# Kernel optimization log

Hardware: AMD Instinct MI355X
Metric: run time of the kernel (lower is better)

## Reference

```python
import jax, jax.numpy as jnp
import numpy as np

D_MODEL = 1024
HIDDEN = 4096
N_EXPERTS = 8
TOP_K = 2


def setup_inputs() -> dict:
    key = jax.random.key(0)
    ks = jax.random.split(key, 7)
    x = jax.random.normal(ks[0], (4, 2048, D_MODEL), dtype=jnp.float32)
    s = 0.02
    Wg = jax.random.normal(ks[1], (D_MODEL, N_EXPERTS), dtype=jnp.float32) * s
    bg = jnp.zeros((N_EXPERTS,), dtype=jnp.float32)
    W1 = jax.random.normal(ks[2], (N_EXPERTS, D_MODEL, HIDDEN), dtype=jnp.float32) * s
    b1 = jnp.zeros((N_EXPERTS, HIDDEN), dtype=jnp.float32)
    W2 = jax.random.normal(ks[3], (N_EXPERTS, HIDDEN, D_MODEL), dtype=jnp.float32) * s
    b2 = jnp.zeros((N_EXPERTS, D_MODEL), dtype=jnp.float32)
    return {"x": x, "Wg": Wg, "bg": bg, "W1": W1, "b1": b1, "W2": W2, "b2": b2}


def reference(x, Wg, bg, W1, b1, W2, b2):
    B, T, D = x.shape
    xf = x.reshape(-1, D)                      # (N, D)
    N = xf.shape[0]

    # --- top-k gate ---
    logits = xf @ Wg + bg                      # (N, E)
    all_probs = jax.nn.softmax(logits, axis=-1)
    topk_logits, topk_idx = jax.lax.top_k(logits, TOP_K)   # (N, k)
    topk_gates = jax.nn.softmax(topk_logits, axis=-1)      # (N, k), sums to 1

    # scatter gates into dense (N, E) masks (matches torch scatter_add_)
    rows = jnp.arange(N)[:, None]
    gate_mask = jnp.zeros((N, N_EXPERTS), dtype=xf.dtype).at[rows, topk_idx].add(topk_gates)
    dispatch_mask = jnp.zeros((N, N_EXPERTS), dtype=xf.dtype).at[rows, topk_idx].add(1.0)

    # --- experts: dense batched form; unselected tokens have gate 0 so math matches ---
    h = jnp.einsum('nd,edh->neh', xf, W1) + b1             # (N, E, H)
    h = jax.nn.relu(h)
    y = jnp.einsum('neh,ehd->ned', h, W2) + b2             # (N, E, D)
    out = jnp.einsum('ned,ne->nd', y, gate_mask)           # weighted combine
    outputs = out.reshape(B, T, D)

    # --- load-balance loss + metadata ---
    tokens_per_expert = (dispatch_mask > 0).sum(axis=0)
    assignment_fraction = gate_mask.sum(axis=0) / N
    expected_prob = all_probs.mean(axis=0)
    load_balance_loss = (expected_prob * assignment_fraction).sum() * N_EXPERTS

    return (outputs, load_balance_loss, tokens_per_expert, expected_prob, assignment_fraction)
```

## Files before the change

### kernel.cpp

```cpp
#include <hip/hip_runtime.h>
#include <stdint.h>

#define D_MODEL 1024
#define HID     4096
#define NE      8
#define NTOK    8192
#define NSLOT   (NTOK*2)
#define TM      128
#define MAX_RB  136
#define MPAD    (MAX_RB*TM)
#define HHALF   2048
#define GATE_BLOCKS 256

typedef unsigned short u16;
typedef __attribute__((ext_vector_type(8))) __bf16 bf16x8;
typedef __attribute__((ext_vector_type(4))) float  f32x4;

__device__ __forceinline__ u16 f2bu(float f){
  uint32_t u = __builtin_bit_cast(uint32_t, f);
  uint32_t r = (u + 0x7FFFu + ((u >> 16) & 1u)) >> 16;
  return (u16)r;
}
__device__ __forceinline__ float b2f(u16 v){
  uint32_t u = ((uint32_t)v) << 16;
  return __builtin_bit_cast(float, u);
}

__device__ __forceinline__ void gload16(const u16* src, u16* lds){
  __builtin_amdgcn_global_load_lds((const __attribute__((address_space(1))) void*)src,
                                   (__attribute__((address_space(3))) void*)lds, 16, 0, 0);
}

__device__ __forceinline__ int xcd_swz(int w, int nwg){
  int q = nwg >> 3;
  return (w & 7) * q + (w >> 3);
}

#define WAITV(n) do{ asm volatile("s_waitcnt vmcnt(" #n ")" ::: "memory"); \
                     __builtin_amdgcn_sched_barrier(0); }while(0)
#define BARX()   do{ __builtin_amdgcn_sched_barrier(0); \
                     __builtin_amdgcn_s_barrier(); \
                     __builtin_amdgcn_sched_barrier(0); }while(0)

__global__ __launch_bounds__(256) void transpose_cvt(const float* __restrict__ in,
                                                     u16* __restrict__ out, int R, int C)
{
  __shared__ float tile[64][33];
  int e = blockIdx.z;
  int r0 = blockIdx.y * 64, c0 = blockIdx.x * 32;
  const float* src = in + (size_t)e * R * C;
  u16* dst = out + (size_t)e * R * C;
  int t = threadIdx.x;
  int rr = t >> 3;
  int tc4 = (t & 7) * 4;
#pragma unroll
  for (int p = 0; p < 2; p++){
    int r = rr + p*32;
    float4 v = *(const float4*)(src + (size_t)(r0 + r) * C + c0 + tc4);
    tile[r][tc4+0] = v.x; tile[r][tc4+1] = v.y;
    tile[r][tc4+2] = v.z; tile[r][tc4+3] = v.w;
  }
  __syncthreads();
  int c = t >> 3;
  int seg = (t & 7) * 8;
  u16 o[8];
#pragma unroll
  for (int j = 0; j < 8; j++) o[j] = f2bu(tile[seg + j][c]);
  *(int4*)(dst + (size_t)(c0 + c) * R + r0 + seg) = *(int4*)o;
}

__global__ __launch_bounds__(256) void gate_kernel(
    const float* __restrict__ x, const float* __restrict__ Wg, const float* __restrict__ bg,
    int* __restrict__ topk, float* __restrict__ gates, u16* __restrict__ x16,
    float* __restrict__ part_probs, float* __restrict__ part_assign, int* __restrict__ part_cnt)
{
  __shared__ float sp[32][8];
  __shared__ float sa[32][8];
  __shared__ int   sc[32][8];
  int t = threadIdx.x;
  int tb = t >> 3;
  int g  = t & 7;
  int n  = blockIdx.x * 32 + tb;
  const float* xr = x + (size_t)n * D_MODEL;
  u16* xo = x16 + (size_t)n * D_MODEL;
  float lg[8];
#pragma unroll
  for (int e = 0; e < 8; e++) lg[e] = 0.f;
  for (int k = 0; k < 32; k++){
    int off = k*32 + g*4;
    float4 v = *(const float4*)(xr + off);
    const float* wr = Wg + (size_t)off * 8;
#pragma unroll
    for (int e = 0; e < 8; e++)
      lg[e] += v.x*wr[e] + v.y*wr[8+e] + v.z*wr[16+e] + v.w*wr[24+e];
    u16 o[4] = {f2bu(v.x), f2bu(v.y), f2bu(v.z), f2bu(v.w)};
    *(uint2*)(xo + off) = *(const uint2*)o;
  }
#pragma unroll
  for (int m = 1; m < 8; m <<= 1)
#pragma unroll
    for (int e = 0; e < 8; e++) lg[e] += __shfl_xor(lg[e], m);
#pragma unroll
  for (int e = 0; e < 8; e++) lg[e] += bg[e];

  float mx = lg[0];
#pragma unroll
  for (int e = 1; e < 8; e++) mx = fmaxf(mx, lg[e]);
  float p[8]; float s = 0.f;
#pragma unroll
  for (int e = 0; e < 8; e++){ p[e] = expf(lg[e]-mx); s += p[e]; }
  float inv = 1.f / s;
  int bi = 0; float best = lg[0];
#pragma unroll
  for (int e = 1; e < 8; e++) if (lg[e] > best){ best = lg[e]; bi = e; }
  int bi2 = 0; float best2 = -3.0e38f;
#pragma unroll
  for (int e = 0; e < 8; e++) if (e != bi && lg[e] > best2){ best2 = lg[e]; bi2 = e; }
  float t1 = expf(best2 - best);
  float g0 = 1.f / (1.f + t1);
  float g1 = t1 / (1.f + t1);
  if (g == 0){
    topk[2*n] = bi;  topk[2*n+1] = bi2;
    gates[2*n] = g0; gates[2*n+1] = g1;
#pragma unroll
    for (int e = 0; e < 8; e++){
      sp[tb][e] = p[e] * inv;
      sa[tb][e] = (e == bi) ? g0 : ((e == bi2) ? g1 : 0.f);
      sc[tb][e] = (e == bi || e == bi2) ? 1 : 0;
    }
  }
  __syncthreads();
  if (t < 8){
    float s2 = 0.f; for (int i = 0; i < 32; i++) s2 += sp[i][t];
    part_probs[blockIdx.x*8 + t] = s2;
  } else if (t < 16){
    int e = t - 8; float s2 = 0.f; for (int i = 0; i < 32; i++) s2 += sa[i][e];
    part_assign[blockIdx.x*8 + e] = s2;
  } else if (t < 24){
    int e = t - 16; int c = 0; for (int i = 0; i < 32; i++) c += sc[i][e];
    part_cnt[blockIdx.x*8 + e] = c;
  }
}

__global__ __launch_bounds__(256) void scan_kernel(const int* __restrict__ part_cnt,
                                                   int* __restrict__ counts,
                                                   int* __restrict__ padded_off,
                                                   int* __restrict__ cursor,
                                                   int* __restrict__ block_expert,
                                                   int* __restrict__ routed)
{
  __shared__ int off[NE+1];
  int t = threadIdx.x;
  if (t == 0){
    int o = 0; off[0] = 0;
    for (int e = 0; e < NE; e++){
      int c = 0;
      for (int b = 0; b < GATE_BLOCKS; b++) c += part_cnt[b*8 + e];
      counts[e] = c;
      o += ((c + TM - 1) / TM) * TM;
      off[e+1] = o;
    }
    for (int e = 0; e <= NE; e++) padded_off[e] = off[e];
  }
  __syncthreads();
  if (t < NE) cursor[t] = 0;
  for (int rb = t; rb < MAX_RB; rb += 256){
    int e = -1;
    int r = rb * TM;
    for (int j = 0; j < NE; j++)
      if (r >= off[j] && r < off[j+1]) e = j;
    block_expert[rb] = e;
  }
  for (int i = t; i < MPAD; i += 256) routed[i] = -1;
}

__global__ __launch_bounds__(256) void place_kernel(const int* __restrict__ topk,
                                                    const int* __restrict__ padded_off,
                                                    int* __restrict__ cursor,
                                                    int* __restrict__ routed)
{
  int s = blockIdx.x * 256 + threadIdx.x;
  int e = topk[s];
  int pos = padded_off[e] + atomicAdd(&cursor[e], 1);
  routed[pos] = s;
}


__global__ __launch_bounds__(256, 3) void gemm1_kernel(
    const u16* __restrict__ x16, const u16* __restrict__ w1t, const float* __restrict__ b1,
    const int* __restrict__ routed, const int* __restrict__ block_expert,
    u16* __restrict__ h, int half)
{
  int l = xcd_swz(blockIdx.x, gridDim.x);
  int rb = l >> 4, cb = l & 15;
  int e = block_expert[rb];
  if (e < 0) return;
  __shared__ __align__(16) u16 Al[3][128][32];
  __shared__ __align__(16) u16 Bl[3][128][32];
  u16* AF = &Al[0][0][0];
  u16* BF = &Bl[0][0][0];
  int t = threadIdx.x;
  int lane = t & 63, wid = t >> 6;

  int srow0 = wid*32 + (lane >> 2);
  int sch = ((lane & 3) ^ ((lane >> 3) & 3)) * 8;

  int slot0 = routed[rb*TM + srow0];
  int slot1 = routed[rb*TM + srow0 + 16];
  int tok0 = slot0 >= 0 ? (slot0 >> 1) : 0;
  int tok1 = slot1 >= 0 ? (slot1 >> 1) : 0;
  const u16* srcA0 = x16 + (size_t)tok0 * D_MODEL + sch;
  const u16* srcA1 = x16 + (size_t)tok1 * D_MODEL + sch;
  const u16* wb = w1t + ((size_t)e*HID + (size_t)half*HHALF + (size_t)cb*128) * D_MODEL + sch;
  const u16* srcB0 = wb + (size_t)srow0 * D_MODEL;
  const u16* srcB1 = wb + (size_t)(srow0 + 16) * D_MODEL;

  int wr = wid >> 1, wc = wid & 1;
  int fr = lane & 15, fk = lane >> 4;
  int fkx8 = (fk ^ ((fr >> 1) & 3)) * 8;
  f32x4 acc[4][4];
#pragma unroll
  for (int i = 0; i < 4; i++)
#pragma unroll
    for (int j = 0; j < 4; j++) acc[i][j] = (f32x4){0.f,0.f,0.f,0.f};

#define STG1(bo, kk) do{ \
    gload16(srcA0 + (kk), AF + (bo) + wid*1024); \
    gload16(srcA1 + (kk), AF + (bo) + wid*1024 + 512); \
    gload16(srcB0 + (kk), BF + (bo) + wid*1024); \
    gload16(srcB1 + (kk), BF + (bo) + wid*1024 + 512); } while(0)

#define CMP1(bo) do{ \
    bf16x8 af[4], bf[4]; \
    _Pragma("unroll") \
    for (int mm = 0; mm < 4; mm++) af[mm] = *(const bf16x8*)(AF + (bo) + (wr*64 + mm*16 + fr)*32 + fkx8); \
    _Pragma("unroll") \
    for (int nn = 0; nn < 4; nn++) bf[nn] = *(const bf16x8*)(BF + (bo) + (wc*64 + nn*16 + fr)*32 + fkx8); \
    _Pragma("unroll") \
    for (int mm = 0; mm < 4; mm++) \
      _Pragma("unroll") \
      for (int nn = 0; nn < 4; nn++) \
        acc[mm][nn] = __builtin_amdgcn_mfma_f32_16x16x32_bf16(af[mm], bf[nn], acc[mm][nn], 0, 0, 0); } while(0)

  const int nk = D_MODEL/32;
  STG1(0, 0); STG1(4096, 32); STG1(8192, 64);
  int bo = 0;
  for (int i = 0; i < nk - 2; i++){
    WAITV(8);
    BARX();
    CMP1(bo);
    BARX();
    if (i < nk - 3) STG1(bo, (i+3)*32);
    bo = (bo == 8192) ? 0 : bo + 4096;
  }
  WAITV(4); BARX(); CMP1(bo); BARX();
  bo = (bo == 8192) ? 0 : bo + 4096;
  WAITV(0); BARX(); CMP1(bo);

  int r4 = fk * 4;
#pragma unroll
  for (int nn = 0; nn < 4; nn++){
    int ct = wc*64 + nn*16 + fr;
    float bias = b1[(size_t)e*HID + (size_t)half*HHALF + cb*128 + ct];
#pragma unroll
    for (int mm = 0; mm < 4; mm++){
#pragma unroll
      for (int r = 0; r < 4; r++){
        int rt = wr*64 + mm*16 + r4 + r;
        float v = acc[mm][nn][r] + bias;
        v = v > 0.f ? v : 0.f;
        h[(size_t)(rb*TM + rt) * HHALF + cb*128 + ct] = f2bu(v);
      }
    }
  }
#undef STG1
#undef CMP1
}

__global__ __launch_bounds__(256, 3) void gemm2_kernel(
    const u16* __restrict__ h, const u16* __restrict__ w2t,
    const int* __restrict__ routed, const int* __restrict__ block_expert,
    const float* __restrict__ gates, u16* __restrict__ y, int half)
{
  int l = xcd_swz(blockIdx.x, gridDim.x);
  int rb = l >> 3, cb = l & 7;
  int e = block_expert[rb];
  if (e < 0) return;
  __shared__ __align__(16) u16 Al[3][128][32];
  __shared__ __align__(16) u16 Bl[3][128][32];
  __shared__ int   rslot[128];
  __shared__ float rgate[128];
  u16* AF = &Al[0][0][0];
  u16* BF = &Bl[0][0][0];
  int t = threadIdx.x;
  int lane = t & 63, wid = t >> 6;
  if (t < 128){
    int s = routed[rb*TM + t];
    rslot[t] = s;
    rgate[t] = (s >= 0) ? gates[s] : 0.f;
  }

  int srow0 = wid*32 + (lane >> 2);
  int sch = ((lane & 3) ^ ((lane >> 3) & 3)) * 8;
  const u16* srcA0 = h + (size_t)(rb*TM + srow0) * HHALF + sch;
  const u16* srcA1 = h + (size_t)(rb*TM + srow0 + 16) * HHALF + sch;
  const u16* wb = w2t + ((size_t)e*D_MODEL + (size_t)cb*128) * HID + (size_t)half*HHALF + sch;
  const u16* srcB0 = wb + (size_t)srow0 * HID;
  const u16* srcB1 = wb + (size_t)(srow0 + 16) * HID;

  int wr = wid >> 1, wc = wid & 1;
  int fr = lane & 15, fk = lane >> 4;
  int fkx8 = (fk ^ ((fr >> 1) & 3)) * 8;
  f32x4 acc[4][4];
#pragma unroll
  for (int i = 0; i < 4; i++)
#pragma unroll
    for (int j = 0; j < 4; j++) acc[i][j] = (f32x4){0.f,0.f,0.f,0.f};

#define STG2(bo, kk) do{ \
    gload16(srcA0 + (kk), AF + (bo) + wid*1024); \
    gload16(srcA1 + (kk), AF + (bo) + wid*1024 + 512); \
    gload16(srcB0 + (kk), BF + (bo) + wid*1024); \
    gload16(srcB1 + (kk), BF + (bo) + wid*1024 + 512); } while(0)

#define CMP2(bo) do{ \
    bf16x8 af[4], bf[4]; \
    _Pragma("unroll") \
    for (int mm = 0; mm < 4; mm++) af[mm] = *(const bf16x8*)(AF + (bo) + (wr*64 + mm*16 + fr)*32 + fkx8); \
    _Pragma("unroll") \
    for (int nn = 0; nn < 4; nn++) bf[nn] = *(const bf16x8*)(BF + (bo) + (wc*64 + nn*16 + fr)*32 + fkx8); \
    _Pragma("unroll") \
    for (int mm = 0; mm < 4; mm++) \
      _Pragma("unroll") \
      for (int nn = 0; nn < 4; nn++) \
        acc[mm][nn] = __builtin_amdgcn_mfma_f32_16x16x32_bf16(af[mm], bf[nn], acc[mm][nn], 0, 0, 0); } while(0)

  const int nk = HHALF/32;
  STG2(0, 0); STG2(4096, 32); STG2(8192, 64);
  int bo = 0;
  for (int i = 0; i < nk - 2; i++){
    WAITV(8);
    BARX();
    CMP2(bo);
    BARX();
    if (i < nk - 3) STG2(bo, (i+3)*32);
    bo = (bo == 8192) ? 0 : bo + 4096;
  }
  WAITV(4); BARX(); CMP2(bo); BARX();
  bo = (bo == 8192) ? 0 : bo + 4096;
  WAITV(0); BARX(); CMP2(bo);

  int r4 = fk * 4;
#pragma unroll
  for (int mm = 0; mm < 4; mm++){
#pragma unroll
    for (int r = 0; r < 4; r++){
      int rt = wr*64 + mm*16 + r4 + r;
      int slot = rslot[rt];
      if (slot < 0) continue;
      float g = rgate[rt];
#pragma unroll
      for (int nn = 0; nn < 4; nn++){
        int ct = wc*64 + nn*16 + fr;
        size_t idx = (size_t)slot * D_MODEL + cb*128 + ct;
        float val = g * acc[mm][nn][r];
        if (half == 0) y[idx] = f2bu(val);
        else           y[idx] = f2bu(b2f(y[idx]) + val);
      }
    }
  }
#undef STG2
#undef CMP2
}

__global__ __launch_bounds__(256) void combine_kernel(
    const u16* __restrict__ y, const int* __restrict__ topk, const float* __restrict__ gates,
    const float* __restrict__ b2, float* __restrict__ out)
{
  int i = blockIdx.x * 256 + threadIdx.x;
  int n = i >> 8;
  int d = (i & 255) * 4;
  ushort4 a4 = *(const ushort4*)(y + (size_t)(2*n)   * D_MODEL + d);
  ushort4 b4 = *(const ushort4*)(y + (size_t)(2*n+1) * D_MODEL + d);
  int e0 = topk[2*n], e1 = topk[2*n+1];
  float g0 = gates[2*n], g1 = gates[2*n+1];
  float4 c0 = *(const float4*)(b2 + (size_t)e0 * D_MODEL + d);
  float4 c1 = *(const float4*)(b2 + (size_t)e1 * D_MODEL + d);
  float4 o;
  o.x = b2f(a4.x) + b2f(b4.x) + g0*c0.x + g1*c1.x;
  o.y = b2f(a4.y) + b2f(b4.y) + g0*c0.y + g1*c1.y;
  o.z = b2f(a4.z) + b2f(b4.z) + g0*c0.z + g1*c1.z;
  o.w = b2f(a4.w) + b2f(b4.w) + g0*c0.w + g1*c1.w;
  *(float4*)(out + (size_t)n * D_MODEL + d) = o;
}

__global__ void finalize_kernel(const float* __restrict__ part_probs,
                                const float* __restrict__ part_assign,
                                const int* __restrict__ counts,
                                float* __restrict__ out_tail)
{
  __shared__ float ep[8], af[8];
  int t = threadIdx.x;
  if (t < 8){
    float s = 0.f;
    for (int b = 0; b < GATE_BLOCKS; b++) s += part_probs[b*8 + t];
    ep[t] = s / (float)NTOK;
  } else if (t < 16){
    int e = t - 8; float s = 0.f;
    for (int b = 0; b < GATE_BLOCKS; b++) s += part_assign[b*8 + e];
    af[e] = s / (float)NTOK;
  }
  __syncthreads();
  if (t == 0){
    float loss = 0.f;
    for (int e = 0; e < 8; e++) loss += ep[e] * af[e];
    out_tail[0] = loss * (float)NE;
  }
  if (t < 8){
    out_tail[1 + t]  = (float)counts[t];
    out_tail[9 + t]  = ep[t];
    out_tail[17 + t] = af[t];
  }
}

extern "C" void kernel_launch(void* const* d_in, const int* in_sizes, int n_in,
                              void* d_out, int out_size, void* d_ws, size_t ws_size,
                              hipStream_t stream)
{
  const float* x  = (const float*)d_in[0];
  const float* Wg = (const float*)d_in[1];
  const float* bg = (const float*)d_in[2];
  const float* W1 = (const float*)d_in[3];
  const float* b1 = (const float*)d_in[4];
  const float* W2 = (const float*)d_in[5];
  const float* b2 = (const float*)d_in[6];
  float* out = (float*)d_out;

  char* ws = (char*)d_ws;
  size_t o = 0;
  auto alloc = [&](size_t bytes) -> char* {
    char* p = ws + o; o = (o + bytes + 255) & ~(size_t)255; return p;
  };
  int*   topk        = (int*)   alloc((size_t)NSLOT*4);
  float* gates       = (float*) alloc((size_t)NSLOT*4);
  int*   counts      = (int*)   alloc(NE*4);
  int*   padded_off  = (int*)   alloc((NE+1)*4);
  int*   cursor      = (int*)   alloc(NE*4);
  int*   block_exp   = (int*)   alloc(MAX_RB*4);
  int*   routed      = (int*)   alloc((size_t)MPAD*4);
  float* part_probs  = (float*) alloc(GATE_BLOCKS*8*4);
  float* part_assign = (float*) alloc(GATE_BLOCKS*8*4);
  int*   part_cnt    = (int*)   alloc(GATE_BLOCKS*8*4);
  u16*   x16         = (u16*)   alloc((size_t)NTOK*D_MODEL*2);
  u16*   w1t         = (u16*)   alloc((size_t)NE*HID*D_MODEL*2);
  u16*   w2t         = (u16*)   alloc((size_t)NE*HID*D_MODEL*2);
  u16*   hbuf        = (u16*)   alloc((size_t)MPAD*HHALF*2);
  u16*   ybuf        = (u16*)   alloc((size_t)NSLOT*D_MODEL*2);
  (void)ws_size; (void)in_sizes; (void)n_in; (void)out_size;

  transpose_cvt<<<dim3(HID/32, D_MODEL/64, NE), 256, 0, stream>>>(W1, w1t, D_MODEL, HID);
  transpose_cvt<<<dim3(D_MODEL/32, HID/64, NE), 256, 0, stream>>>(W2, w2t, HID, D_MODEL);
  gate_kernel<<<GATE_BLOCKS, 256, 0, stream>>>(x, Wg, bg, topk, gates, x16, part_probs, part_assign, part_cnt);
  scan_kernel<<<1, 256, 0, stream>>>(part_cnt, counts, padded_off, cursor, block_exp, routed);
  place_kernel<<<NSLOT/256, 256, 0, stream>>>(topk, padded_off, cursor, routed);
  for (int half = 0; half < 2; half++){
    gemm1_kernel<<<16*MAX_RB, 256, 0, stream>>>(x16, w1t, b1, routed, block_exp, hbuf, half);
    gemm2_kernel<<<8*MAX_RB, 256, 0, stream>>>(hbuf, w2t, routed, block_exp, gates, ybuf, half);
  }
  combine_kernel<<<NTOK, 256, 0, stream>>>(ybuf, topk, gates, b2, out);
  finalize_kernel<<<1, 64, 0, stream>>>(part_probs, part_assign, counts, out + (size_t)NTOK*D_MODEL);
}
```

Before: 661.9 us.

## Merge weight transposes with gate kernel and double-buffer GEMMs for occupancy

Folds the two weight transpose/convert launches and the gate kernel into one prep_kernel that dispatches on block index, removing two launches and letting gate work overlap the transposes. Both expert GEMM kernels drop from a 3-stage to a 2-stage LDS pipeline and raise the launch-bounds occupancy hint from 3 to 5 blocks per CU. The smaller LDS footprint and higher occupancy are meant to hide latency through more resident waves, at the cost of less prefetch depth per block and possible register pressure.

```diff
diff --git a/kernel.cpp b/kernel.cpp
--- a/kernel.cpp
+++ b/kernel.cpp
@@ -42,45 +42,55 @@
                      __builtin_amdgcn_s_barrier(); \
                      __builtin_amdgcn_sched_barrier(0); }while(0)
 
-__global__ __launch_bounds__(256) void transpose_cvt(const float* __restrict__ in,
-                                                     u16* __restrict__ out, int R, int C)
-{
-  __shared__ float tile[64][33];
-  int e = blockIdx.z;
-  int r0 = blockIdx.y * 64, c0 = blockIdx.x * 32;
-  const float* src = in + (size_t)e * R * C;
-  u16* dst = out + (size_t)e * R * C;
-  int t = threadIdx.x;
-  int rr = t >> 3;
-  int tc4 = (t & 7) * 4;
-#pragma unroll
-  for (int p = 0; p < 2; p++){
-    int r = rr + p*32;
-    float4 v = *(const float4*)(src + (size_t)(r0 + r) * C + c0 + tc4);
-    tile[r][tc4+0] = v.x; tile[r][tc4+1] = v.y;
-    tile[r][tc4+2] = v.z; tile[r][tc4+3] = v.w;
-  }
-  __syncthreads();
-  int c = t >> 3;
-  int seg = (t & 7) * 8;
-  u16 o[8];
-#pragma unroll
-  for (int j = 0; j < 8; j++) o[j] = f2bu(tile[seg + j][c]);
-  *(int4*)(dst + (size_t)(c0 + c) * R + r0 + seg) = *(int4*)o;
-}
-
-__global__ __launch_bounds__(256) void gate_kernel(
+__global__ __launch_bounds__(256) void prep_kernel(
     const float* __restrict__ x, const float* __restrict__ Wg, const float* __restrict__ bg,
+    const float* __restrict__ W1, const float* __restrict__ W2,
+    u16* __restrict__ w1t, u16* __restrict__ w2t,
     int* __restrict__ topk, float* __restrict__ gates, u16* __restrict__ x16,
     float* __restrict__ part_probs, float* __restrict__ part_assign, int* __restrict__ part_cnt)
 {
+  int id = blockIdx.x;
+  int t = threadIdx.x;
+  if (id < 32768){
+    __shared__ float tile[64][33];
+    const float* in; u16* out; int R, C, r0, c0, e;
+    if (id < 16384){
+      int bx = id & 127, by = (id >> 7) & 15; e = id >> 11;
+      R = D_MODEL; C = HID; r0 = by*64; c0 = bx*32;
+      in = W1; out = w1t;
+    } else {
+      int j = id - 16384;
+      int bx = j & 31, by = (j >> 5) & 63; e = j >> 11;
+      R = HID; C = D_MODEL; r0 = by*64; c0 = bx*32;
+      in = W2; out = w2t;
+    }
+    const float* src = in + (size_t)e * R * C;
+    u16* dst = out + (size_t)e * R * C;
+    int rr = t >> 3;
+    int tc4 = (t & 7) * 4;
+#pragma unroll
+    for (int p = 0; p < 2; p++){
+      int r = rr + p*32;
+      float4 v = *(const float4*)(src + (size_t)(r0 + r) * C + c0 + tc4);
+      tile[r][tc4+0] = v.x; tile[r][tc4+1] = v.y;
+      tile[r][tc4+2] = v.z; tile[r][tc4+3] = v.w;
+    }
+    __syncthreads();
+    int c = t >> 3;
+    int seg = (t & 7) * 8;
+    u16 o[8];
+#pragma unroll
+    for (int j = 0; j < 8; j++) o[j] = f2bu(tile[seg + j][c]);
+    *(int4*)(dst + (size_t)(c0 + c) * R + r0 + seg) = *(int4*)o;
+    return;
+  }
+  int gb = id - 32768;
   __shared__ float sp[32][8];
   __shared__ float sa[32][8];
   __shared__ int   sc[32][8];
-  int t = threadIdx.x;
   int tb = t >> 3;
   int g  = t & 7;
-  int n  = blockIdx.x * 32 + tb;
+  int n  = gb * 32 + tb;
   const float* xr = x + (size_t)n * D_MODEL;
   u16* xo = x16 + (size_t)n * D_MODEL;
   float lg[8];
@@ -132,13 +142,13 @@
   __syncthreads();
   if (t < 8){
     float s2 = 0.f; for (int i = 0; i < 32; i++) s2 += sp[i][t];
-    part_probs[blockIdx.x*8 + t] = s2;
+    part_probs[gb*8 + t] = s2;
   } else if (t < 16){
     int e = t - 8; float s2 = 0.f; for (int i = 0; i < 32; i++) s2 += sa[i][e];
-    part_assign[blockIdx.x*8 + e] = s2;
+    part_assign[gb*8 + e] = s2;
   } else if (t < 24){
     int e = t - 16; int c = 0; for (int i = 0; i < 32; i++) c += sc[i][e];
-    part_cnt[blockIdx.x*8 + e] = c;
+    part_cnt[gb*8 + e] = c;
   }
 }
 
@@ -186,7 +196,7 @@
 }
 
 
-__global__ __launch_bounds__(256, 3) void gemm1_kernel(
+__global__ __launch_bounds__(256, 5) void gemm1_kernel(
     const u16* __restrict__ x16, const u16* __restrict__ w1t, const float* __restrict__ b1,
     const int* __restrict__ routed, const int* __restrict__ block_expert,
     u16* __restrict__ h, int half)
@@ -195,8 +205,8 @@
   int rb = l >> 4, cb = l & 15;
   int e = block_expert[rb];
   if (e < 0) return;
-  __shared__ __align__(16) u16 Al[3][128][32];
-  __shared__ __align__(16) u16 Bl[3][128][32];
+  __shared__ __align__(16) u16 Al[2][128][32];
+  __shared__ __align__(16) u16 Bl[2][128][32];
   u16* AF = &Al[0][0][0];
   u16* BF = &Bl[0][0][0];
   int t = threadIdx.x;
@@ -243,18 +253,16 @@
         acc[mm][nn] = __builtin_amdgcn_mfma_f32_16x16x32_bf16(af[mm], bf[nn], acc[mm][nn], 0, 0, 0); } while(0)
 
   const int nk = D_MODEL/32;
-  STG1(0, 0); STG1(4096, 32); STG1(8192, 64);
+  STG1(0, 0); STG1(4096, 32);
   int bo = 0;
-  for (int i = 0; i < nk - 2; i++){
-    WAITV(8);
+  for (int i = 0; i < nk - 1; i++){
+    WAITV(4);
     BARX();
     CMP1(bo);
     BARX();
-    if (i < nk - 3) STG1(bo, (i+3)*32);
-    bo = (bo == 8192) ? 0 : bo + 4096;
-  }
-  WAITV(4); BARX(); CMP1(bo); BARX();
-  bo = (bo == 8192) ? 0 : bo + 4096;
+    if (i + 2 < nk) STG1(bo, (i+2)*32);
+    bo ^= 4096;
+  }
   WAITV(0); BARX(); CMP1(bo);
 
   int r4 = fk * 4;
@@ -277,7 +285,7 @@
 #undef CMP1
 }
 
-__global__ __launch_bounds__(256, 3) void gemm2_kernel(
+__global__ __launch_bounds__(256, 5) void gemm2_kernel(
     const u16* __restrict__ h, const u16* __restrict__ w2t,
     const int* __restrict__ routed, const int* __restrict__ block_expert,
     const float* __restrict__ gates, u16* __restrict__ y, int half)
@@ -286,8 +294,8 @@
   int rb = l >> 3, cb = l & 7;
   int e = block_expert[rb];
   if (e < 0) return;
-  __shared__ __align__(16) u16 Al[3][128][32];
-  __shared__ __align__(16) u16 Bl[3][128][32];
+  __shared__ __align__(16) u16 Al[2][128][32];
+  __shared__ __align__(16) u16 Bl[2][128][32];
   __shared__ int   rslot[128];
   __shared__ float rgate[128];
   u16* AF = &Al[0][0][0];
@@ -336,18 +344,16 @@
         acc[mm][nn] = __builtin_amdgcn_mfma_f32_16x16x32_bf16(af[mm], bf[nn], acc[mm][nn], 0, 0, 0); } while(0)
 
   const int nk = HHALF/32;
-  STG2(0, 0); STG2(4096, 32); STG2(8192, 64);
+  STG2(0, 0); STG2(4096, 32);
   int bo = 0;
-  for (int i = 0; i < nk - 2; i++){
-    WAITV(8);
+  for (int i = 0; i < nk - 1; i++){
+    WAITV(4);
     BARX();
     CMP2(bo);
     BARX();
-    if (i < nk - 3) STG2(bo, (i+3)*32);
-    bo = (bo == 8192) ? 0 : bo + 4096;
-  }
-  WAITV(4); BARX(); CMP2(bo); BARX();
-  bo = (bo == 8192) ? 0 : bo + 4096;
+    if (i + 2 < nk) STG2(bo, (i+2)*32);
+    bo ^= 4096;
+  }
   WAITV(0); BARX(); CMP2(bo);
 
   int r4 = fk * 4;
@@ -458,9 +464,8 @@
   u16*   ybuf        = (u16*)   alloc((size_t)NSLOT*D_MODEL*2);
   (void)ws_size; (void)in_sizes; (void)n_in; (void)out_size;
 
-  transpose_cvt<<<dim3(HID/32, D_MODEL/64, NE), 256, 0, stream>>>(W1, w1t, D_MODEL, HID);
-  transpose_cvt<<<dim3(D_MODEL/32, HID/64, NE), 256, 0, stream>>>(W2, w2t, HID, D_MODEL);
-  gate_kernel<<<GATE_BLOCKS, 256, 0, stream>>>(x, Wg, bg, topk, gates, x16, part_probs, part_assign, part_cnt);
+  prep_kernel<<<33024, 256, 0, stream>>>(x, Wg, bg, W1, W2, w1t, w2t,
+                                         topk, gates, x16, part_probs, part_assign, part_cnt);
   scan_kernel<<<1, 256, 0, stream>>>(part_cnt, counts, padded_off, cursor, block_exp, routed);
   place_kernel<<<NSLOT/256, 256, 0, stream>>>(topk, padded_off, cursor, routed);
   for (int half = 0; half < 2; half++){
```

Result: slower. 815.3 us (+23.2%).
